# Kernel optimization log

Measured on AMD Instinct MI355X. Metric: run time of the kernel, lower is better.

Reference implementation:

```python
import jax, jax.numpy as jnp
import numpy as np

D_MODEL = 1024
D_MEM = 256


def setup_inputs() -> dict:
    key = jax.random.key(0)
    ks = jax.random.split(key, 12)
    b, s = 4, 2048
    sc_d = 1.0 / np.sqrt(D_MODEL)
    sc_m = 1.0 / np.sqrt(D_MEM)
    return {
        "x": jax.random.normal(ks[0], (b, s, D_MODEL), dtype=jnp.float32),
        "state": jnp.zeros((b, D_MEM, D_MEM), dtype=jnp.float32),
        "Wk": jax.random.normal(ks[1], (D_MODEL, D_MEM), dtype=jnp.float32) * sc_d,
        "bk": jnp.zeros((D_MEM,), dtype=jnp.float32),
        "Wv": jax.random.normal(ks[2], (D_MODEL, D_MEM), dtype=jnp.float32) * sc_d,
        "bv": jnp.zeros((D_MEM,), dtype=jnp.float32),
        "Wq": jax.random.normal(ks[3], (D_MODEL, D_MEM), dtype=jnp.float32) * sc_d,
        "bq": jnp.zeros((D_MEM,), dtype=jnp.float32),
        "Wo": jax.random.normal(ks[4], (D_MEM, D_MODEL), dtype=jnp.float32) * sc_m,
        "bo": jnp.zeros((D_MODEL,), dtype=jnp.float32),
        "Wg": jax.random.normal(ks[5], (D_MODEL, 1), dtype=jnp.float32) * sc_d,
        "bg": jnp.zeros((1,), dtype=jnp.float32),
        "decay": jnp.float32(0.95),
    }


def reference(x, state, Wk, bk, Wv, bv, Wq, bq, Wo, bo, Wg, bg, decay):
    # projections: [b, s, d_mem]
    k = x @ Wk + bk
    v = x @ Wv + bv
    q = x @ Wq + bq
    surprise = jax.nn.sigmoid(x @ Wg + bg)  # [b, s, 1]

    # time-major for scan: [s, b, ...]
    kT = jnp.swapaxes(k, 0, 1)
    vT = jnp.swapaxes(v, 0, 1)
    qT = jnp.swapaxes(q, 0, 1)
    sT = jnp.swapaxes(surprise, 0, 1)  # [s, b, 1]

    def step(S, inp):
        k_t, v_t, q_t, s_t = inp  # [b,dm],[b,dm],[b,dm],[b,1]
        # read: q_t (row) @ S  -> [b, dm]
        mem_out = jnp.einsum('bd,bde->be', q_t, S)
        # write: decayed rank-1 outer-product update, gated by surprise
        assoc = jnp.einsum('bd,be->bde', v_t, k_t)  # v k^T
        S_new = decay * S + s_t[:, :, None] * assoc
        return S_new, mem_out

    final_state, outs = jax.lax.scan(step, state, (kT, vT, qT, sT))
    outputs = jnp.swapaxes(outs, 0, 1)  # [b, s, dm]
    y = outputs @ Wo + bo  # [b, s, d_model]
    return y, final_state
```

## Files before the change

kernel.cpp:

```cpp
#include <hip/hip_runtime.h>
#include <math.h>


using bf16x8 = __attribute__((ext_vector_type(8))) short;
using f32x4  = __attribute__((ext_vector_type(4))) float;
using u16x4  = __attribute__((ext_vector_type(4))) unsigned short;
using u16x8  = __attribute__((ext_vector_type(8))) unsigned short;

__device__ inline unsigned short f2bf(float f) {
  unsigned int u = __float_as_uint(f);
  u = (u + 0x7FFF + ((u >> 16) & 1)) >> 16;
  return (unsigned short)u;
}
__device__ inline float bf2f(unsigned short u) {
  return __uint_as_float(((unsigned int)u) << 16);
}

#define GLD_LDS(gsrc, ldst) \
  __builtin_amdgcn_global_load_lds( \
      (const __attribute__((address_space(1))) unsigned int*)(gsrc), \
      (__attribute__((address_space(3))) unsigned int*)(ldst), 16, 0, 0)

struct MP {
  const unsigned short* A; long long a_bs; int lda;
  const unsigned short* B; long long b_bs; int ldb;
  int K, grid_n;
  int swz;
  float* Cf; unsigned short* Cb; long long c_bs; int ldc;
  const float* bias0; const float* bias1; const float* bias2;
  const float* decay_ptr;
  const float* gate;
  unsigned short* o_v; unsigned short* o_qd;
  unsigned short* o_kT; unsigned short* o_vTw;
};

template<int EPI>
__global__ __launch_bounds__(256)
void gemm_mfma(MP p) {
  __shared__ unsigned short smem[2 * 128 * 64];
  __shared__ float warr[128];
  unsigned short* As = smem;
  unsigned short* Bs = smem + 128 * 64;
  const int tid = threadIdx.x;
  const int bid = p.swz ? ((blockIdx.x & 7) * (gridDim.x >> 3) + (blockIdx.x >> 3))
                        : blockIdx.x;
  const int bn = bid % p.grid_n, bm = bid / p.grid_n;
  const int m0 = bm * 128, n0 = bn * 128;
  const long long z = blockIdx.z;
  const int lane = tid & 63, wv = tid >> 6;
  const int wr = wv >> 1, wc = wv & 1;
  const int srow = tid >> 3, scol = (tid & 7) * 8;

  f32x4 acc[4][4] = {};

  const unsigned short* Abase = p.A + z * p.a_bs + (long long)m0 * p.lda;
  const unsigned short* Bbase = p.B + z * p.b_bs + (long long)n0 * p.ldb;

  for (int k0 = 0; k0 < p.K; k0 += 64) {
    if (k0) __syncthreads();
#pragma unroll
    for (int i = 0; i < 4; i++) {
      int row = i * 32 + srow;
      GLD_LDS(Abase + (long long)row * p.lda + k0 + scol, &As[row * 64 + scol]);
    }
#pragma unroll
    for (int i = 0; i < 4; i++) {
      int row = i * 32 + srow;
      GLD_LDS(Bbase + (long long)row * p.ldb + k0 + scol, &Bs[row * 64 + scol]);
    }
    __syncthreads();
#pragma unroll
    for (int kk = 0; kk < 2; kk++) {
      bf16x8 af[4], bfr[4];
      const int kb = kk * 32 + 8 * (lane >> 4);
#pragma unroll
      for (int m = 0; m < 4; m++)
        af[m] = *(const bf16x8*)&As[(wr * 64 + m * 16 + (lane & 15)) * 64 + kb];
#pragma unroll
      for (int n = 0; n < 4; n++)
        bfr[n] = *(const bf16x8*)&Bs[(wc * 64 + n * 16 + (lane & 15)) * 64 + kb];
#pragma unroll
      for (int m = 0; m < 4; m++)
#pragma unroll
        for (int n = 0; n < 4; n++)
          acc[m][n] = __builtin_amdgcn_mfma_f32_16x16x32_bf16(af[m], bfr[n], acc[m][n], 0, 0, 0);
    }
  }

  if (EPI == 1 || EPI == 4) {
    const int crow0 = m0 + wr * 64, ccol0 = n0 + wc * 64;
#pragma unroll
    for (int m = 0; m < 4; m++) {
#pragma unroll
      for (int n = 0; n < 4; n++) {
        int col = ccol0 + n * 16 + (lane & 15);
#pragma unroll
        for (int q = 0; q < 4; q++) {
          int row = crow0 + m * 16 + (lane >> 4) * 4 + q;
          float v = acc[m][n][q];
          if (EPI == 1) p.Cf[(long long)row * p.ldc + col] = v + p.bias0[col];
          else          p.Cb[z * p.c_bs + (long long)row * p.ldc + col] = f2bf(v);
        }
      }
    }
    return;
  }

  const float log2d = log2f(p.decay_ptr[0]);
  const int sel = bn >> 1;
  const int half = bn & 1;

  if (sel < 2) {
    __syncthreads();
    if (sel == 1 && tid < 128)
      warr[tid] = p.gate[(long long)bm * 128 + tid] * exp2f((float)(127 - tid) * log2d);
  }

#pragma unroll
  for (int m = 0; m < 4; m++) {
#pragma unroll
    for (int n = 0; n < 4; n++) {
      int cl = wc * 64 + n * 16 + (lane & 15);
      int d = half * 128 + cl;
      float bias;
      if (sel == 0) bias = p.bias0[d];
      else if (sel == 1) bias = p.bias1[d];
      else bias = p.bias2[(n0 + cl) - 512];
      int r0 = wr * 64 + m * 16 + (lane >> 4) * 4;
      if (sel < 2) {
        u16x4 pk;
#pragma unroll
        for (int q = 0; q < 4; q++) {
          float v = acc[m][n][q] + bias;
          pk[q] = f2bf(v);
          if (sel == 1) {
            long long row = m0 + r0 + q;
            p.o_v[row * 256 + d] = pk[q];
          }
        }
        int byteoff = (cl * 256 + r0 * 2) ^ ((cl & 7) << 4);
        *(u16x4*)((char*)smem + byteoff) = pk;
      } else {
#pragma unroll
        for (int q = 0; q < 4; q++) {
          long long row = m0 + r0 + q;
          float v = acc[m][n][q] + bias;
          p.o_qd[row * 256 + ((n0 + cl) - 512)] = f2bf(v * exp2f((float)((r0 + q) & 127) * log2d));
        }
      }
    }
  }

  if (sel < 2) {
    __syncthreads();
    unsigned short* dst = (sel == 0 ? p.o_kT : p.o_vTw) + (long long)bm * 32768;
#pragma unroll
    for (int pp = 0; pp < 8; pp++) {
      int idx = pp * 256 + tid;
      int c = idx >> 4;
      int j0 = (idx & 15) * 8;
      u16x8 o = *(const u16x8*)((char*)smem + ((c * 256 + j0 * 2) ^ ((c & 7) << 4)));
      if (sel == 1) {
#pragma unroll
        for (int t = 0; t < 8; t++) o[t] = f2bf(bf2f(o[t]) * warr[j0 + t]);
      }
      *(u16x8*)&dst[(long long)(half * 128 + c) * 128 + j0] = o;
    }
  }
}

__global__ __launch_bounds__(512)
void chunk_attn(const unsigned short* __restrict__ qd16, const unsigned short* __restrict__ v16,
                const unsigned short* __restrict__ kT16, const unsigned short* __restrict__ T16,
                unsigned short* __restrict__ mo16, const float* __restrict__ gbuf,
                const float* __restrict__ decay_ptr) {
  __shared__ unsigned short As[64 * 64];
  __shared__ unsigned short Bs[2 * 128 * 64];
  __shared__ unsigned short Al[64 * 128];
  const int tid = threadIdx.x, lane = tid & 63, wv = tid >> 6;
  const int wr = wv >> 2, wc = wv & 3;
  const int nh = blockIdx.x, rh = blockIdx.y, z = blockIdx.z;
  const int roff = rh * 64;
  const int srow = tid >> 3, scol = (tid & 7) * 8;
  const float log2d = log2f(decay_ptr[0]);

  const unsigned short* qz = qd16 + (long long)z * 32768 + (long long)roff * 256;
  const unsigned short* vz = v16 + (long long)z * 32768;
  const unsigned short* Tz = T16 + (long long)z * 65536 + (long long)nh * 128 * 256;
  const unsigned short* kz = kT16 + (long long)z * 32768 + (long long)nh * 128 * 128;

  f32x4 acc1[2][2] = {};
  f32x4 acc2[2][2] = {};

  for (int k0 = 0; k0 < 256; k0 += 64) {
    if (k0) __syncthreads();
    GLD_LDS(qz + (long long)srow * 256 + k0 + scol, &As[srow * 64 + scol]);
#pragma unroll
    for (int i = 0; i < 2; i++) {
      int row = i * 64 + srow;
      GLD_LDS(vz + (long long)row * 256 + k0 + scol, &Bs[row * 64 + scol]);
      GLD_LDS(Tz + (long long)row * 256 + k0 + scol, &Bs[8192 + row * 64 + scol]);
    }
    __syncthreads();
#pragma unroll
    for (int kk = 0; kk < 2; kk++) {
      const int kb = kk * 32 + 8 * (lane >> 4);
      bf16x8 af[2], bv[2], bt[2];
#pragma unroll
      for (int m = 0; m < 2; m++)
        af[m] = *(const bf16x8*)&As[(wr * 32 + m * 16 + (lane & 15)) * 64 + kb];
#pragma unroll
      for (int n = 0; n < 2; n++) {
        bv[n] = *(const bf16x8*)&Bs[(wc * 32 + n * 16 + (lane & 15)) * 64 + kb];
        bt[n] = *(const bf16x8*)&Bs[8192 + (wc * 32 + n * 16 + (lane & 15)) * 64 + kb];
      }
#pragma unroll
      for (int m = 0; m < 2; m++)
#pragma unroll
        for (int n = 0; n < 2; n++) {
          acc1[m][n] = __builtin_amdgcn_mfma_f32_16x16x32_bf16(af[m], bv[n], acc1[m][n], 0, 0, 0);
          acc2[m][n] = __builtin_amdgcn_mfma_f32_16x16x32_bf16(af[m], bt[n], acc2[m][n], 0, 0, 0);
        }
    }
  }

#pragma unroll
  for (int n = 0; n < 2; n++) {
    int col = wc * 32 + n * 16 + (lane & 15);
    float gsc = gbuf[z * 128 + col] * exp2f(-(float)(col + 1) * log2d);
#pragma unroll
    for (int m = 0; m < 2; m++) {
#pragma unroll
      for (int q = 0; q < 4; q++) {
        int r = wr * 32 + m * 16 + (lane >> 4) * 4 + q;
        float v = (col < roff + r) ? acc1[m][n][q] * gsc : 0.f;
        int byteoff = (r * 256 + col * 2) ^ ((r & 7) << 4);
        *(unsigned short*)((char*)Al + byteoff) = f2bf(v);
      }
    }
  }
  __syncthreads();

  for (int k0 = 0; k0 < 128; k0 += 64) {
    if (k0) __syncthreads();
#pragma unroll
    for (int i = 0; i < 2; i++) {
      int row = i * 64 + srow;
      GLD_LDS(kz + (long long)row * 128 + k0 + scol, &Bs[row * 64 + scol]);
    }
    __syncthreads();
#pragma unroll
    for (int kk = 0; kk < 2; kk++) {
      const int kbb = k0 + kk * 32 + 8 * (lane >> 4);
      bf16x8 af[2], bk_[2];
#pragma unroll
      for (int m = 0; m < 2; m++) {
        int r = wr * 32 + m * 16 + (lane & 15);
        af[m] = *(const bf16x8*)((char*)Al + ((r * 256 + kbb * 2) ^ ((r & 7) << 4)));
      }
#pragma unroll
      for (int n = 0; n < 2; n++)
        bk_[n] = *(const bf16x8*)&Bs[(wc * 32 + n * 16 + (lane & 15)) * 64 + kk * 32 + 8 * (lane >> 4)];
#pragma unroll
      for (int m = 0; m < 2; m++)
#pragma unroll
        for (int n = 0; n < 2; n++)
          acc2[m][n] = __builtin_amdgcn_mfma_f32_16x16x32_bf16(af[m], bk_[n], acc2[m][n], 0, 0, 0);
    }
  }

#pragma unroll
  for (int m = 0; m < 2; m++) {
#pragma unroll
    for (int n = 0; n < 2; n++) {
      int col = nh * 128 + wc * 32 + n * 16 + (lane & 15);
#pragma unroll
      for (int q = 0; q < 4; q++) {
        int row = roff + wr * 32 + m * 16 + (lane >> 4) * 4 + q;
        mo16[((long long)z * 128 + row) * 256 + col] = f2bf(acc2[m][n][q]);
      }
    }
  }
}

__global__ __launch_bounds__(256)
void prep_kernel(const float* __restrict__ x, const float* __restrict__ Wg,
                 const float* __restrict__ bg, unsigned short* __restrict__ x16,
                 float* __restrict__ g,
                 const float* __restrict__ Wk, const float* __restrict__ Wv,
                 const float* __restrict__ Wq, unsigned short* __restrict__ w16,
                 const float* __restrict__ Wo, unsigned short* __restrict__ wot16) {
  __shared__ float tile[64][65];
  const int bx = blockIdx.x;
  const int tid = threadIdx.x;
  if (bx < 2048) {
    const int wave = tid >> 6, lane = tid & 63;
    const long long row = (long long)bx * 4 + wave;
    const float* xr = x + row * 1024 + lane * 16;
    const float* wr = Wg + lane * 16;
    float s = 0.f;
    u16x8 o0, o1;
#pragma unroll
    for (int qq = 0; qq < 2; qq++) {
      float4 a = *(const float4*)(xr + qq * 4);
      float4 w = *(const float4*)(wr + qq * 4);
      s = fmaf(a.x, w.x, s); s = fmaf(a.y, w.y, s);
      s = fmaf(a.z, w.z, s); s = fmaf(a.w, w.w, s);
      o0[qq * 4 + 0] = f2bf(a.x); o0[qq * 4 + 1] = f2bf(a.y);
      o0[qq * 4 + 2] = f2bf(a.z); o0[qq * 4 + 3] = f2bf(a.w);
    }
#pragma unroll
    for (int qq = 0; qq < 2; qq++) {
      float4 a = *(const float4*)(xr + 8 + qq * 4);
      float4 w = *(const float4*)(wr + 8 + qq * 4);
      s = fmaf(a.x, w.x, s); s = fmaf(a.y, w.y, s);
      s = fmaf(a.z, w.z, s); s = fmaf(a.w, w.w, s);
      o1[qq * 4 + 0] = f2bf(a.x); o1[qq * 4 + 1] = f2bf(a.y);
      o1[qq * 4 + 2] = f2bf(a.z); o1[qq * 4 + 3] = f2bf(a.w);
    }
    *(u16x8*)(x16 + row * 1024 + lane * 16) = o0;
    *(u16x8*)(x16 + row * 1024 + lane * 16 + 8) = o1;
#pragma unroll
    for (int off = 32; off; off >>= 1) s += __shfl_xor(s, off, 64);
    if (lane == 0) g[row] = 1.f / (1.f + expf(-(s + bg[0])));
    return;
  }
  int t = bx - 2048;
  const float* S; unsigned short* dst;
  int srcCols, dstLd, k0, n0g, n0;
  if (t < 192) {
    k0 = (t % 16) * 64; n0g = (t / 16) * 64;
    int sel = n0g >> 8; n0 = n0g - (sel << 8);
    S = sel == 0 ? Wk : sel == 1 ? Wv : Wq;
    srcCols = 256; dst = w16; dstLd = 1024;
  } else {
    t -= 192;
    k0 = (t % 4) * 64; n0g = (t / 4) * 64; n0 = n0g;
    S = Wo; srcCols = 1024; dst = wot16; dstLd = 256;
  }
  const int rr = tid >> 4, c4 = (tid & 15) * 4;
#pragma unroll
  for (int pp = 0; pp < 4; pp++) {
    int r = pp * 16 + rr;
    float4 v = *(const float4*)&S[(long long)(k0 + r) * srcCols + n0 + c4];
    tile[r][c4 + 0] = v.x; tile[r][c4 + 1] = v.y; tile[r][c4 + 2] = v.z; tile[r][c4 + 3] = v.w;
  }
  __syncthreads();
  const int rn = tid >> 3, ck0 = (tid & 7) * 8;
#pragma unroll
  for (int pp = 0; pp < 2; pp++) {
    int n = pp * 32 + rn;
    u16x8 o;
#pragma unroll
    for (int j = 0; j < 8; j++) o[j] = f2bf(tile[ck0 + j][n]);
    *(u16x8*)&dst[(long long)(n0g + n) * dstLd + k0 + ck0] = o;
  }
}

__global__ __launch_bounds__(256)
void scan_kernel(const unsigned short* __restrict__ Ut16, const float* __restrict__ state_in,
                 unsigned short* __restrict__ T16, float* __restrict__ final_out,
                 const float* __restrict__ decay_ptr) {
  int t = blockIdx.x * 256 + threadIdx.x;
  int b = t >> 16, pidx = t & 65535;
  int e = pidx >> 8, d = pidx & 255;
  float dC = exp2f(128.f * log2f(decay_ptr[0]));
  float cur = state_in[(long long)b * 65536 + d * 256 + e];
#pragma unroll
  for (int c = 0; c < 16; c++) {
    long long off = ((long long)(b * 16 + c)) * 65536 + pidx;
    T16[off] = f2bf(cur);
    cur = fmaf(dC, cur, bf2f(Ut16[off]));
  }
  final_out[(long long)b * 65536 + d * 256 + e] = cur;
}

extern "C" void kernel_launch(void* const* d_in, const int* in_sizes, int n_in,
                              void* d_out, int out_size, void* d_ws, size_t ws_size,
                              hipStream_t stream) {
  const float* x     = (const float*)d_in[0];
  const float* state = (const float*)d_in[1];
  const float* Wk = (const float*)d_in[2];  const float* bk = (const float*)d_in[3];
  const float* Wv = (const float*)d_in[4];  const float* bv = (const float*)d_in[5];
  const float* Wq = (const float*)d_in[6];  const float* bq = (const float*)d_in[7];
  const float* Wo = (const float*)d_in[8];  const float* bo = (const float*)d_in[9];
  const float* Wg = (const float*)d_in[10]; const float* bg = (const float*)d_in[11];
  const float* decay = (const float*)d_in[12];

  float* out_y = (float*)d_out;
  float* out_S = out_y + 8388608;

  float* ws = (float*)d_ws;
  unsigned short* x16   = (unsigned short*)(ws);
  unsigned short* v16   = (unsigned short*)(ws + 4194304);
  unsigned short* qd16  = (unsigned short*)(ws + 5242880);
  unsigned short* w16   = (unsigned short*)(ws + 6291456);
  unsigned short* wot16 = (unsigned short*)(ws + 6684672);
  float*          gbuf  = ws + 6815744;
  unsigned short* kT16  = (unsigned short*)(ws + 6823936);
  unsigned short* vTw16 = (unsigned short*)(ws + 7872512);
  unsigned short* Ut16  = (unsigned short*)(ws + 8921088);
  unsigned short* T16   = (unsigned short*)(ws + 11018240);
  unsigned short* mo16  = (unsigned short*)(ws + 13115392);

  prep_kernel<<<2304, 256, 0, stream>>>(x, Wg, bg, x16, gbuf, Wk, Wv, Wq, w16, Wo, wot16);

  {
    MP p{};
    p.A = x16; p.lda = 1024; p.B = w16; p.ldb = 1024;
    p.K = 1024; p.grid_n = 6; p.swz = 1;
    p.bias0 = bk; p.bias1 = bv; p.bias2 = bq;
    p.decay_ptr = decay; p.gate = gbuf;
    p.o_v = v16; p.o_qd = qd16; p.o_kT = kT16; p.o_vTw = vTw16;
    gemm_mfma<0><<<dim3(384, 1, 1), 256, 0, stream>>>(p);
  }

  {
    MP p{};
    p.A = kT16;  p.a_bs = 32768; p.lda = 128;
    p.B = vTw16; p.b_bs = 32768; p.ldb = 128;
    p.K = 128; p.grid_n = 2; p.swz = 0;
    p.Cb = Ut16; p.c_bs = 65536; p.ldc = 256;
    p.decay_ptr = decay;
    gemm_mfma<4><<<dim3(4, 1, 64), 256, 0, stream>>>(p);
  }

  scan_kernel<<<1024, 256, 0, stream>>>(Ut16, state, T16, out_S, decay);

  chunk_attn<<<dim3(2, 2, 64), 512, 0, stream>>>(qd16, v16, kT16, T16, mo16, gbuf, decay);

  {
    MP p{};
    p.A = mo16; p.lda = 256;
    p.B = wot16; p.ldb = 256;
    p.K = 256; p.grid_n = 8; p.swz = 1;
    p.Cf = out_y; p.ldc = 1024;
    p.bias0 = bo; p.decay_ptr = decay;
    gemm_mfma<1><<<dim3(512, 1, 1), 256, 0, stream>>>(p);
  }
}
```

Before: 93.55 us.

## Fuse chunk-state GEMM, scan and chunk attention into one cooperative kernel

Replaces three separate launches (the batched Ut GEMM, the inter-chunk scan, and chunk_attn) with one cooperative kernel of 256 blocks that uses grid-wide syncs between phases. The aim is to remove kernel launch gaps and tail effects between these small phases. In exchange it adds the cost of grid.sync, forces all blocks to be co-resident at 512 threads each, and changes the tile shape of the Ut GEMM phase.

```diff
diff --git a/kernel.cpp b/kernel.cpp
--- a/kernel.cpp
+++ b/kernel.cpp
@@ -1,6 +1,9 @@
 #include <hip/hip_runtime.h>
+#include <hip/hip_cooperative_groups.h>
 #include <math.h>
 
+
+namespace cg = cooperative_groups;
 
 using bf16x8 = __attribute__((ext_vector_type(8))) short;
 using f32x4  = __attribute__((ext_vector_type(4))) float;
@@ -46,15 +49,14 @@
                         : blockIdx.x;
   const int bn = bid % p.grid_n, bm = bid / p.grid_n;
   const int m0 = bm * 128, n0 = bn * 128;
-  const long long z = blockIdx.z;
   const int lane = tid & 63, wv = tid >> 6;
   const int wr = wv >> 1, wc = wv & 1;
   const int srow = tid >> 3, scol = (tid & 7) * 8;
 
   f32x4 acc[4][4] = {};
 
-  const unsigned short* Abase = p.A + z * p.a_bs + (long long)m0 * p.lda;
-  const unsigned short* Bbase = p.B + z * p.b_bs + (long long)n0 * p.ldb;
+  const unsigned short* Abase = p.A + (long long)m0 * p.lda;
+  const unsigned short* Bbase = p.B + (long long)n0 * p.ldb;
 
   for (int k0 = 0; k0 < p.K; k0 += 64) {
     if (k0) __syncthreads();
@@ -87,7 +89,7 @@
     }
   }
 
-  if (EPI == 1 || EPI == 4) {
+  if (EPI == 1) {
     const int crow0 = m0 + wr * 64, ccol0 = n0 + wc * 64;
 #pragma unroll
     for (int m = 0; m < 4; m++) {
@@ -97,9 +99,7 @@
 #pragma unroll
         for (int q = 0; q < 4; q++) {
           int row = crow0 + m * 16 + (lane >> 4) * 4 + q;
-          float v = acc[m][n][q];
-          if (EPI == 1) p.Cf[(long long)row * p.ldc + col] = v + p.bias0[col];
-          else          p.Cb[z * p.c_bs + (long long)row * p.ldc + col] = f2bf(v);
+          p.Cf[(long long)row * p.ldc + col] = acc[m][n][q] + p.bias0[col];
         }
       }
     }
@@ -170,114 +170,200 @@
 }
 
 __global__ __launch_bounds__(512)
-void chunk_attn(const unsigned short* __restrict__ qd16, const unsigned short* __restrict__ v16,
-                const unsigned short* __restrict__ kT16, const unsigned short* __restrict__ T16,
-                unsigned short* __restrict__ mo16, const float* __restrict__ gbuf,
-                const float* __restrict__ decay_ptr) {
-  __shared__ unsigned short As[64 * 64];
-  __shared__ unsigned short Bs[2 * 128 * 64];
-  __shared__ unsigned short Al[64 * 128];
+void tail_kernel(const unsigned short* __restrict__ kT16, const unsigned short* __restrict__ vTw16,
+                 unsigned short* __restrict__ Ut16, const float* __restrict__ state_in,
+                 unsigned short* __restrict__ T16, float* __restrict__ final_out,
+                 const unsigned short* __restrict__ qd16, const unsigned short* __restrict__ v16,
+                 unsigned short* __restrict__ mo16, const float* __restrict__ gbuf,
+                 const float* __restrict__ decay_ptr) {
+  __shared__ unsigned short pool[28672];
+  cg::grid_group grid = cg::this_grid();
   const int tid = threadIdx.x, lane = tid & 63, wv = tid >> 6;
-  const int wr = wv >> 2, wc = wv & 3;
-  const int nh = blockIdx.x, rh = blockIdx.y, z = blockIdx.z;
-  const int roff = rh * 64;
-  const int srow = tid >> 3, scol = (tid & 7) * 8;
+  const int bid = blockIdx.x;
+  const int z = bid >> 2;
   const float log2d = log2f(decay_ptr[0]);
 
-  const unsigned short* qz = qd16 + (long long)z * 32768 + (long long)roff * 256;
-  const unsigned short* vz = v16 + (long long)z * 32768;
-  const unsigned short* Tz = T16 + (long long)z * 65536 + (long long)nh * 128 * 256;
-  const unsigned short* kz = kT16 + (long long)z * 32768 + (long long)nh * 128 * 128;
-
-  f32x4 acc1[2][2] = {};
-  f32x4 acc2[2][2] = {};
-
-  for (int k0 = 0; k0 < 256; k0 += 64) {
-    if (k0) __syncthreads();
-    GLD_LDS(qz + (long long)srow * 256 + k0 + scol, &As[srow * 64 + scol]);
-#pragma unroll
-    for (int i = 0; i < 2; i++) {
-      int row = i * 64 + srow;
-      GLD_LDS(vz + (long long)row * 256 + k0 + scol, &Bs[row * 64 + scol]);
-      GLD_LDS(Tz + (long long)row * 256 + k0 + scol, &Bs[8192 + row * 64 + scol]);
-    }
+  {
+    unsigned short* As = pool;
+    unsigned short* Bs = pool + 8192;
+    const int eh = (bid >> 1) & 1, dh = bid & 1;
+    const int e0 = eh * 128, d0 = dh * 128;
+    const int wr = wv >> 2, wc = wv & 3;
+    const int srow = tid >> 3, scol = (tid & 7) * 8;
+    const unsigned short* kz = kT16 + (long long)z * 32768;
+    const unsigned short* vz = vTw16 + (long long)z * 32768;
+    f32x4 acc[4][2] = {};
+    for (int k0 = 0; k0 < 128; k0 += 64) {
+      if (k0) __syncthreads();
+#pragma unroll
+      for (int i = 0; i < 2; i++) {
+        int row = i * 64 + srow;
+        GLD_LDS(kz + (long long)(e0 + row) * 128 + k0 + scol, &As[row * 64 + scol]);
+        GLD_LDS(vz + (long long)(d0 + row) * 128 + k0 + scol, &Bs[row * 64 + scol]);
+      }
+      __syncthreads();
+#pragma unroll
+      for (int kk = 0; kk < 2; kk++) {
+        const int kb = kk * 32 + 8 * (lane >> 4);
+        bf16x8 af[4], bfr[2];
+#pragma unroll
+        for (int m = 0; m < 4; m++)
+          af[m] = *(const bf16x8*)&As[(wr * 64 + m * 16 + (lane & 15)) * 64 + kb];
+#pragma unroll
+        for (int n = 0; n < 2; n++)
+          bfr[n] = *(const bf16x8*)&Bs[(wc * 32 + n * 16 + (lane & 15)) * 64 + kb];
+#pragma unroll
+        for (int m = 0; m < 4; m++)
+#pragma unroll
+          for (int n = 0; n < 2; n++)
+            acc[m][n] = __builtin_amdgcn_mfma_f32_16x16x32_bf16(af[m], bfr[n], acc[m][n], 0, 0, 0);
+      }
+    }
+#pragma unroll
+    for (int m = 0; m < 4; m++) {
+#pragma unroll
+      for (int n = 0; n < 2; n++) {
+        int col = d0 + wc * 32 + n * 16 + (lane & 15);
+#pragma unroll
+        for (int q = 0; q < 4; q++) {
+          int row = e0 + wr * 64 + m * 16 + (lane >> 4) * 4 + q;
+          Ut16[(long long)z * 65536 + (long long)row * 256 + col] = f2bf(acc[m][n][q]);
+        }
+      }
+    }
+  }
+
+  __threadfence();
+  grid.sync();
+
+  {
+    float dC = exp2f(128.f * log2d);
+    int t0 = bid * 512 + tid;
+#pragma unroll
+    for (int h = 0; h < 2; h++) {
+      int t = t0 + h * 131072;
+      int b = t >> 16, pidx = t & 65535;
+      int e = pidx >> 8, d = pidx & 255;
+      float cur = state_in[(long long)b * 65536 + d * 256 + e];
+#pragma unroll
+      for (int c = 0; c < 16; c++) {
+        long long off = ((long long)(b * 16 + c)) * 65536 + pidx;
+        T16[off] = f2bf(cur);
+        cur = fmaf(dC, cur, bf2f(Ut16[off]));
+      }
+      final_out[(long long)b * 65536 + d * 256 + e] = cur;
+    }
+  }
+
+  __threadfence();
+  grid.sync();
+
+  {
+    unsigned short* As = pool;
+    unsigned short* Bs = pool + 4096;
+    unsigned short* Al = pool + 4096 + 16384;
+    const int nh = bid & 1, rh = (bid >> 1) & 1;
+    const int roff = rh * 64;
+    const int wr = wv >> 2, wc = wv & 3;
+    const int srow = tid >> 3, scol = (tid & 7) * 8;
+
+    const unsigned short* qz = qd16 + (long long)z * 32768 + (long long)roff * 256;
+    const unsigned short* vz = v16 + (long long)z * 32768;
+    const unsigned short* Tz = T16 + (long long)z * 65536 + (long long)nh * 128 * 256;
+    const unsigned short* kz = kT16 + (long long)z * 32768 + (long long)nh * 128 * 128;
+
+    f32x4 acc1[2][2] = {};
+    f32x4 acc2[2][2] = {};
+
     __syncthreads();
-#pragma unroll
-    for (int kk = 0; kk < 2; kk++) {
-      const int kb = kk * 32 + 8 * (lane >> 4);
-      bf16x8 af[2], bv[2], bt[2];
-#pragma unroll
-      for (int m = 0; m < 2; m++)
-        af[m] = *(const bf16x8*)&As[(wr * 32 + m * 16 + (lane & 15)) * 64 + kb];
+
+    for (int k0 = 0; k0 < 256; k0 += 64) {
+      if (k0) __syncthreads();
+      GLD_LDS(qz + (long long)srow * 256 + k0 + scol, &As[srow * 64 + scol]);
+#pragma unroll
+      for (int i = 0; i < 2; i++) {
+        int row = i * 64 + srow;
+        GLD_LDS(vz + (long long)row * 256 + k0 + scol, &Bs[row * 64 + scol]);
+        GLD_LDS(Tz + (long long)row * 256 + k0 + scol, &Bs[8192 + row * 64 + scol]);
+      }
+      __syncthreads();
+#pragma unroll
+      for (int kk = 0; kk < 2; kk++) {
+        const int kb = kk * 32 + 8 * (lane >> 4);
+        bf16x8 af[2], bv[2], bt[2];
+#pragma unroll
+        for (int m = 0; m < 2; m++)
+          af[m] = *(const bf16x8*)&As[(wr * 32 + m * 16 + (lane & 15)) * 64 + kb];
+#pragma unroll
+        for (int n = 0; n < 2; n++) {
+          bv[n] = *(const bf16x8*)&Bs[(wc * 32 + n * 16 + (lane & 15)) * 64 + kb];
+          bt[n] = *(const bf16x8*)&Bs[8192 + (wc * 32 + n * 16 + (lane & 15)) * 64 + kb];
+        }
+#pragma unroll
+        for (int m = 0; m < 2; m++)
+#pragma unroll
+          for (int n = 0; n < 2; n++) {
+            acc1[m][n] = __builtin_amdgcn_mfma_f32_16x16x32_bf16(af[m], bv[n], acc1[m][n], 0, 0, 0);
+            acc2[m][n] = __builtin_amdgcn_mfma_f32_16x16x32_bf16(af[m], bt[n], acc2[m][n], 0, 0, 0);
+          }
+      }
+    }
+
+#pragma unroll
+    for (int n = 0; n < 2; n++) {
+      int col = wc * 32 + n * 16 + (lane & 15);
+      float gsc = gbuf[z * 128 + col] * exp2f(-(float)(col + 1) * log2d);
+#pragma unroll
+      for (int m = 0; m < 2; m++) {
+#pragma unroll
+        for (int q = 0; q < 4; q++) {
+          int r = wr * 32 + m * 16 + (lane >> 4) * 4 + q;
+          float v = (col < roff + r) ? acc1[m][n][q] * gsc : 0.f;
+          int byteoff = (r * 256 + col * 2) ^ ((r & 7) << 4);
+          *(unsigned short*)((char*)Al + byteoff) = f2bf(v);
+        }
+      }
+    }
+    __syncthreads();
+
+    for (int k0 = 0; k0 < 128; k0 += 64) {
+      if (k0) __syncthreads();
+#pragma unroll
+      for (int i = 0; i < 2; i++) {
+        int row = i * 64 + srow;
+        GLD_LDS(kz + (long long)row * 128 + k0 + scol, &Bs[row * 64 + scol]);
+      }
+      __syncthreads();
+#pragma unroll
+      for (int kk = 0; kk < 2; kk++) {
+        const int kbb = k0 + kk * 32 + 8 * (lane >> 4);
+        bf16x8 af[2], bk_[2];
+#pragma unroll
+        for (int m = 0; m < 2; m++) {
+          int r = wr * 32 + m * 16 + (lane & 15);
+          af[m] = *(const bf16x8*)((char*)Al + ((r * 256 + kbb * 2) ^ ((r & 7) << 4)));
+        }
+#pragma unroll
+        for (int n = 0; n < 2; n++)
+          bk_[n] = *(const bf16x8*)&Bs[(wc * 32 + n * 16 + (lane & 15)) * 64 + kk * 32 + 8 * (lane >> 4)];
+#pragma unroll
+        for (int m = 0; m < 2; m++)
+#pragma unroll
+          for (int n = 0; n < 2; n++)
+            acc2[m][n] = __builtin_amdgcn_mfma_f32_16x16x32_bf16(af[m], bk_[n], acc2[m][n], 0, 0, 0);
+      }
+    }
+
+#pragma unroll
+    for (int m = 0; m < 2; m++) {
 #pragma unroll
       for (int n = 0; n < 2; n++) {
-        bv[n] = *(const bf16x8*)&Bs[(wc * 32 + n * 16 + (lane & 15)) * 64 + kb];
-        bt[n] = *(const bf16x8*)&Bs[8192 + (wc * 32 + n * 16 + (lane & 15)) * 64 + kb];
-      }
-#pragma unroll
-      for (int m = 0; m < 2; m++)
-#pragma unroll
-        for (int n = 0; n < 2; n++) {
-          acc1[m][n] = __builtin_amdgcn_mfma_f32_16x16x32_bf16(af[m], bv[n], acc1[m][n], 0, 0, 0);
-          acc2[m][n] = __builtin_amdgcn_mfma_f32_16x16x32_bf16(af[m], bt[n], acc2[m][n], 0, 0, 0);
-        }
-    }
-  }
-
-#pragma unroll
-  for (int n = 0; n < 2; n++) {
-    int col = wc * 32 + n * 16 + (lane & 15);
-    float gsc = gbuf[z * 128 + col] * exp2f(-(float)(col + 1) * log2d);
-#pragma unroll
-    for (int m = 0; m < 2; m++) {
-#pragma unroll
-      for (int q = 0; q < 4; q++) {
-        int r = wr * 32 + m * 16 + (lane >> 4) * 4 + q;
-        float v = (col < roff + r) ? acc1[m][n][q] * gsc : 0.f;
-        int byteoff = (r * 256 + col * 2) ^ ((r & 7) << 4);
-        *(unsigned short*)((char*)Al + byteoff) = f2bf(v);
-      }
-    }
-  }
-  __syncthreads();
-
-  for (int k0 = 0; k0 < 128; k0 += 64) {
-    if (k0) __syncthreads();
-#pragma unroll
-    for (int i = 0; i < 2; i++) {
-      int row = i * 64 + srow;
-      GLD_LDS(kz + (long long)row * 128 + k0 + scol, &Bs[row * 64 + scol]);
-    }
-    __syncthreads();
-#pragma unroll
-    for (int kk = 0; kk < 2; kk++) {
-      const int kbb = k0 + kk * 32 + 8 * (lane >> 4);
-      bf16x8 af[2], bk_[2];
-#pragma unroll
-      for (int m = 0; m < 2; m++) {
-        int r = wr * 32 + m * 16 + (lane & 15);
-        af[m] = *(const bf16x8*)((char*)Al + ((r * 256 + kbb * 2) ^ ((r & 7) << 4)));
-      }
-#pragma unroll
-      for (int n = 0; n < 2; n++)
-        bk_[n] = *(const bf16x8*)&Bs[(wc * 32 + n * 16 + (lane & 15)) * 64 + kk * 32 + 8 * (lane >> 4)];
-#pragma unroll
-      for (int m = 0; m < 2; m++)
-#pragma unroll
-        for (int n = 0; n < 2; n++)
-          acc2[m][n] = __builtin_amdgcn_mfma_f32_16x16x32_bf16(af[m], bk_[n], acc2[m][n], 0, 0, 0);
-    }
-  }
-
-#pragma unroll
-  for (int m = 0; m < 2; m++) {
-#pragma unroll
-    for (int n = 0; n < 2; n++) {
-      int col = nh * 128 + wc * 32 + n * 16 + (lane & 15);
-#pragma unroll
-      for (int q = 0; q < 4; q++) {
-        int row = roff + wr * 32 + m * 16 + (lane >> 4) * 4 + q;
-        mo16[((long long)z * 128 + row) * 256 + col] = f2bf(acc2[m][n][q]);
+        int col = nh * 128 + wc * 32 + n * 16 + (lane & 15);
+#pragma unroll
+        for (int q = 0; q < 4; q++) {
+          int row = roff + wr * 32 + m * 16 + (lane >> 4) * 4 + q;
+          mo16[((long long)z * 128 + row) * 256 + col] = f2bf(acc2[m][n][q]);
+        }
       }
     }
   }
@@ -357,24 +443,6 @@
   }
 }
 
-__global__ __launch_bounds__(256)
-void scan_kernel(const unsigned short* __restrict__ Ut16, const float* __restrict__ state_in,
-                 unsigned short* __restrict__ T16, float* __restrict__ final_out,
-                 const float* __restrict__ decay_ptr) {
-  int t = blockIdx.x * 256 + threadIdx.x;
-  int b = t >> 16, pidx = t & 65535;
-  int e = pidx >> 8, d = pidx & 255;
-  float dC = exp2f(128.f * log2f(decay_ptr[0]));
-  float cur = state_in[(long long)b * 65536 + d * 256 + e];
-#pragma unroll
-  for (int c = 0; c < 16; c++) {
-    long long off = ((long long)(b * 16 + c)) * 65536 + pidx;
-    T16[off] = f2bf(cur);
-    cur = fmaf(dC, cur, bf2f(Ut16[off]));
-  }
-  final_out[(long long)b * 65536 + d * 256 + e] = cur;
-}
-
 extern "C" void kernel_launch(void* const* d_in, const int* in_sizes, int n_in,
                               void* d_out, int out_size, void* d_ws, size_t ws_size,
                               hipStream_t stream) {
@@ -416,18 +484,16 @@
   }
 
   {
-    MP p{};
-    p.A = kT16;  p.a_bs = 32768; p.lda = 128;
-    p.B = vTw16; p.b_bs = 32768; p.ldb = 128;
-    p.K = 128; p.grid_n = 2; p.swz = 0;
-    p.Cb = Ut16; p.c_bs = 65536; p.ldc = 256;
-    p.decay_ptr = decay;
-    gemm_mfma<4><<<dim3(4, 1, 64), 256, 0, stream>>>(p);
-  }
-
-  scan_kernel<<<1024, 256, 0, stream>>>(Ut16, state, T16, out_S, decay);
-
-  chunk_attn<<<dim3(2, 2, 64), 512, 0, stream>>>(qd16, v16, kT16, T16, mo16, gbuf, decay);
+    const unsigned short* a_kT = kT16; const unsigned short* a_vTw = vTw16;
+    unsigned short* a_Ut = Ut16; const float* a_state = state;
+    unsigned short* a_T = T16; float* a_final = out_S;
+    const unsigned short* a_qd = qd16; const unsigned short* a_v = v16;
+    unsigned short* a_mo = mo16; const float* a_g = gbuf; const float* a_d = decay;
+    void* kargs[] = {&a_kT, &a_vTw, &a_Ut, &a_state, &a_T, &a_final,
+                     &a_qd, &a_v, &a_mo, &a_g, &a_d};
+    hipLaunchCooperativeKernel((void*)tail_kernel, dim3(256, 1, 1), dim3(512, 1, 1),
+                               kargs, 0, stream);
+  }
 
   {
     MP p{};
```

Result: slower. 302.1 us (+223.0%).
